# Performance work log

Measured on AMD Instinct MI355X. Metric: run time of the kernel, lower is better.

The kernel has to match this reference:

```python
import jax, jax.numpy as jnp
import numpy as np

NUM_GRAPHS = 32
NODES_PER_GRAPH = 256
N = NUM_GRAPHS * NODES_PER_GRAPH
IN_CH, HID, OUT_CH = 64, 256, 32
K = 20
SPACE, PROP = 3, 2
NEG_SLOPE = 0.01  # F.leaky_relu default
BIG = 1e9         # cross-graph distance mask


def _glorot(key, shape):
    fan_in, fan_out = shape
    lim = (6.0 / (fan_in + fan_out)) ** 0.5
    return jax.random.uniform(key, shape, jnp.float32, -lim, lim)


def setup_inputs() -> dict:
    key = jax.random.key(0)
    ks = jax.random.split(key, 16)
    inp = {
        "x": jax.random.normal(ks[0], (N, IN_CH), jnp.float32),
        "batch": jnp.repeat(jnp.arange(NUM_GRAPHS, dtype=jnp.int32), NODES_PER_GRAPH),
    }
    dims = [(IN_CH, HID), (HID, HID), (HID, OUT_CH)]
    i = 1
    for li, (cin, cout) in enumerate(dims, start=1):
        inp[f"Ws{li}"] = _glorot(ks[i], (cin, SPACE)); i += 1
        inp[f"bs{li}"] = jnp.zeros((SPACE,), jnp.float32)
        inp[f"Wh{li}"] = _glorot(ks[i], (cin, PROP)); i += 1
        inp[f"bh{li}"] = jnp.zeros((PROP,), jnp.float32)
        inp[f"Wo{li}"] = _glorot(ks[i], (cin + PROP, cout)); i += 1
        inp[f"bo{li}"] = jnp.zeros((cout,), jnp.float32)
    return inp


def gravnet_conv(x, mask_add, Ws, bs, Wh, bh, Wo, bo):
    s = x @ Ws + bs                                     # [N,3] learned coords
    h = x @ Wh + bh                                     # [N,2] propagate feats
    s2 = jnp.sum(s * s, axis=1)
    d2 = s2[:, None] + s2[None, :] - 2.0 * (s @ s.T)    # [N,N] squared dists
    d2 = jnp.maximum(d2, 0.0) + mask_add                # block within-graph only
    neg_d2, idx = jax.lax.top_k(-d2, K)                 # kNN (includes self)
    w = jnp.exp(10.0 * neg_d2)                          # exp(-10 * d^2)
    agg = jnp.einsum('nk,nkp->np', w, h[idx])           # aggr='add'
    return jnp.concatenate([agg, x], axis=-1) @ Wo + bo  # lin(cat([out, x]))


def _leaky(h):
    return jnp.where(h >= 0, h, NEG_SLOPE * h)


def reference(x, batch,
              Ws1, bs1, Wh1, bh1, Wo1, bo1,
              Ws2, bs2, Wh2, bh2, Wo2, bo2,
              Ws3, bs3, Wh3, bh3, Wo3, bo3):
    mask_add = jnp.where(batch[:, None] == batch[None, :], 0.0, BIG).astype(x.dtype)
    # dropout p=0.0 -> identity
    h = _leaky(gravnet_conv(x, mask_add, Ws1, bs1, Wh1, bh1, Wo1, bo1))
    h = _leaky(gravnet_conv(h, mask_add, Ws2, bs2, Wh2, bh2, Wo2, bo2))
    out = gravnet_conv(h, mask_add, Ws3, bs3, Wh3, bh3, Wo3, bo3)
    # get_zero_nodes: first node of each contiguous graph segment
    b = jnp.concatenate([jnp.zeros((1,), batch.dtype), batch])
    diff = (b[1:] - b[:-1]).at[0].set(1)
    first_idx = jnp.nonzero(diff != 0, size=NUM_GRAPHS)[0]
    return out[first_idx]
```

## Files before the change

kernel.cpp:

```cpp
#include <hip/hip_runtime.h>
#include <hip/hip_bf16.h>


#define NGRAPH 32
#define GN 256
#define NTOT (NGRAPH*GN)
#define KNN 20
#define CTS 129

typedef __attribute__((ext_vector_type(8))) short bf16x8;
typedef __attribute__((ext_vector_type(4))) float f32x4;

__device__ __forceinline__ ushort f2bf(float x) {
    union { float f; unsigned u; } a; a.f = x;
    unsigned r = a.u + 0x7FFFu + ((a.u >> 16) & 1u);
    return (ushort)(r >> 16);
}
__device__ __forceinline__ float bf2f(ushort h) {
    union { unsigned u; float f; } b; b.u = ((unsigned)h) << 16;
    return b.f;
}
__device__ __forceinline__ bf16x8 ld8(const ushort* p) {
    return *reinterpret_cast<const bf16x8*>(p);
}
__device__ __forceinline__ unsigned pack2(ushort a, ushort b) {
    return (unsigned)a | ((unsigned)b << 16);
}

#define DPP_MIN(v, ctrl, rmask) { \
    unsigned _t = (unsigned)__builtin_amdgcn_update_dpp((int)(v), (int)(v), ctrl, rmask, 0xf, false); \
    (v) = _t < (v) ? _t : (v); }
#define DPP_ADD(v, ctrl, rmask) { \
    float _t = __int_as_float(__builtin_amdgcn_update_dpp(0, __float_as_int(v), ctrl, rmask, 0xf, true)); \
    (v) += _t; }
__device__ __forceinline__ unsigned wave_min_u32(unsigned v) {
    DPP_MIN(v, 0x111, 0xf)
    DPP_MIN(v, 0x112, 0xf)
    DPP_MIN(v, 0x114, 0xf)
    DPP_MIN(v, 0x118, 0xf)
    DPP_MIN(v, 0x142, 0xa)
    DPP_MIN(v, 0x143, 0xc)
    return (unsigned)__builtin_amdgcn_readlane((int)v, 63);
}
__device__ __forceinline__ float wave_sum_f32(float v) {
    DPP_ADD(v, 0x111, 0xf)
    DPP_ADD(v, 0x112, 0xf)
    DPP_ADD(v, 0x114, 0xf)
    DPP_ADD(v, 0x118, 0xf)
    DPP_ADD(v, 0x142, 0xa)
    DPP_ADD(v, 0x143, 0xc)
    return __int_as_float(__builtin_amdgcn_readlane(__float_as_int(v), 63));
}

__device__ __forceinline__ void knn_extract(
    unsigned ua, unsigned ub, unsigned uc, unsigned ud,
    float2 hA, float2 hB, float2 hC, float2 hD,
    int lane, float& out0, float& out1)
{
    float acc0 = 0.f, acc1 = 0.f;
#pragma unroll 1
    for (int it = 0; it < KNN; ++it) {
        unsigned m1 = ua < ub ? ua : ub;
        unsigned m2 = uc < ud ? uc : ud;
        unsigned bv = m1 < m2 ? m1 : m2;
        unsigned gv = wave_min_u32(bv);
        float d2 = __uint_as_float(gv);
        float w = __expf(-10.0f * d2);
        unsigned long long mask = __ballot(bv == gv);
        int wl = __ffsll(mask) - 1;
        if (lane == wl) {
            float h0, h1;
            if (ua == gv)      { h0 = hA.x; h1 = hA.y; ua = 0xFFFFFFFFu; }
            else if (ub == gv) { h0 = hB.x; h1 = hB.y; ub = 0xFFFFFFFFu; }
            else if (uc == gv) { h0 = hC.x; h1 = hC.y; uc = 0xFFFFFFFFu; }
            else               { h0 = hD.x; h1 = hD.y; ud = 0xFFFFFFFFu; }
            acc0 = fmaf(w, h0, acc0);
            acc1 = fmaf(w, h1, acc1);
        }
    }
    out0 = wave_sum_f32(acc0);
    out1 = wave_sum_f32(acc1);
}

__device__ __forceinline__ void knn_rows4(
    const float* sh5, int rbase, int lane, int growbase, float* __restrict__ agg)
{
    float sjx[4], sjy[4], sjz[4], s2j[4];
    float2 hs[4];
#pragma unroll
    for (int t = 0; t < 4; ++t) {
        int j = lane + 64 * t;
        float x = sh5[j * 5 + 0], y = sh5[j * 5 + 1], z = sh5[j * 5 + 2];
        sjx[t] = x; sjy[t] = y; sjz[t] = z;
        s2j[t] = x * x + y * y + z * z;
        hs[t] = make_float2(sh5[j * 5 + 3], sh5[j * 5 + 4]);
    }
    unsigned key[4][4];
    float acc0[4], acc1[4];
#pragma unroll
    for (int r = 0; r < 4; ++r) {
        int rl = rbase + r;
        float s0 = sh5[rl * 5 + 0], s1v = sh5[rl * 5 + 1], s2v = sh5[rl * 5 + 2];
        float s2row = s0 * s0 + s1v * s1v + s2v * s2v;
#pragma unroll
        for (int t = 0; t < 4; ++t) {
            float dot = s0 * sjx[t] + s1v * sjy[t] + s2v * sjz[t];
            float d2 = s2row + s2j[t] - 2.0f * dot;
            key[r][t] = __float_as_uint(d2 > 0.f ? d2 : 0.f);
        }
        acc0[r] = 0.f; acc1[r] = 0.f;
    }
#pragma unroll 1
    for (int it = 0; it < KNN; ++it) {
        unsigned bv[4], gv[4];
#pragma unroll
        for (int r = 0; r < 4; ++r) {
            unsigned m1 = key[r][0] < key[r][1] ? key[r][0] : key[r][1];
            unsigned m2 = key[r][2] < key[r][3] ? key[r][2] : key[r][3];
            bv[r] = m1 < m2 ? m1 : m2;
            gv[r] = bv[r];
        }
#define KSTAGE(ctrl, rmask) { \
        DPP_MIN(gv[0], ctrl, rmask) DPP_MIN(gv[1], ctrl, rmask) \
        DPP_MIN(gv[2], ctrl, rmask) DPP_MIN(gv[3], ctrl, rmask) }
        KSTAGE(0x111, 0xf) KSTAGE(0x112, 0xf) KSTAGE(0x114, 0xf)
        KSTAGE(0x118, 0xf) KSTAGE(0x142, 0xa) KSTAGE(0x143, 0xc)
#undef KSTAGE
#pragma unroll
        for (int r = 0; r < 4; ++r) {
            unsigned g = (unsigned)__builtin_amdgcn_readlane((int)gv[r], 63);
            float w = __expf(-10.0f * __uint_as_float(g));
            unsigned long long mask = __ballot(bv[r] == g);
            int wl = __ffsll(mask) - 1;
            if (lane == wl) {
                float h0, h1;
                if (key[r][0] == g)      { h0 = hs[0].x; h1 = hs[0].y; key[r][0] = 0xFFFFFFFFu; }
                else if (key[r][1] == g) { h0 = hs[1].x; h1 = hs[1].y; key[r][1] = 0xFFFFFFFFu; }
                else if (key[r][2] == g) { h0 = hs[2].x; h1 = hs[2].y; key[r][2] = 0xFFFFFFFFu; }
                else                     { h0 = hs[3].x; h1 = hs[3].y; key[r][3] = 0xFFFFFFFFu; }
                acc0[r] = fmaf(w, h0, acc0[r]);
                acc1[r] = fmaf(w, h1, acc1[r]);
            }
        }
    }
#define SSTAGE(ctrl, rmask) { \
    DPP_ADD(acc0[0], ctrl, rmask) DPP_ADD(acc1[0], ctrl, rmask) \
    DPP_ADD(acc0[1], ctrl, rmask) DPP_ADD(acc1[1], ctrl, rmask) \
    DPP_ADD(acc0[2], ctrl, rmask) DPP_ADD(acc1[2], ctrl, rmask) \
    DPP_ADD(acc0[3], ctrl, rmask) DPP_ADD(acc1[3], ctrl, rmask) }
    SSTAGE(0x111, 0xf) SSTAGE(0x112, 0xf) SSTAGE(0x114, 0xf)
    SSTAGE(0x118, 0xf) SSTAGE(0x142, 0xa) SSTAGE(0x143, 0xc)
#undef SSTAGE
    if (lane == 63) {
#pragma unroll
        for (int r = 0; r < 4; ++r) {
            agg[(growbase + rbase + r) * 2 + 0] = acc0[r];
            agg[(growbase + rbase + r) * 2 + 1] = acc1[r];
        }
    }
}

__global__ __launch_bounds__(256) void knn1_mega(
    const float* __restrict__ X,
    const float* __restrict__ Ws1, const float* __restrict__ bs1,
    const float* __restrict__ Wh1, const float* __restrict__ bh1,
    const float* __restrict__ Wo1, const float* __restrict__ Wo2,
    const float* __restrict__ bs2, const float* __restrict__ bh2,
    const float* __restrict__ bs3, const float* __restrict__ bh3,
    ushort* __restrict__ Wt1hi, ushort* __restrict__ Wt1lo,
    ushort* __restrict__ Wt2hi, ushort* __restrict__ Wt2lo,
    ushort* __restrict__ Xhi, ushort* __restrict__ Xlo,
    float* __restrict__ s2, float* __restrict__ h2p,
    float* __restrict__ s3, float* __restrict__ h3p,
    float* __restrict__ agg)
{
    __shared__ float sh5[256 * 5];
    int b = blockIdx.x, tid = threadIdx.x;
    if (b < 512) {
        int g = b >> 4;
        const float* Xg = X + (size_t)g * (GN * 64);
        {
            float a0 = 0.f, a1 = 0.f, a2 = 0.f, a3 = 0.f, a4 = 0.f;
            const float* xr = Xg + tid * 64;
#pragma unroll 4
            for (int c0 = 0; c0 < 64; c0 += 4) {
                float4 v = *reinterpret_cast<const float4*>(&xr[c0]);
                float xv[4] = {v.x, v.y, v.z, v.w};
#pragma unroll
                for (int j = 0; j < 4; ++j) {
                    int c = c0 + j;
                    a0 = fmaf(xv[j], Ws1[c * 3 + 0], a0);
                    a1 = fmaf(xv[j], Ws1[c * 3 + 1], a1);
                    a2 = fmaf(xv[j], Ws1[c * 3 + 2], a2);
                    a3 = fmaf(xv[j], Wh1[c * 2 + 0], a3);
                    a4 = fmaf(xv[j], Wh1[c * 2 + 1], a4);
                }
            }
            sh5[tid * 5 + 0] = a0 + bs1[0];
            sh5[tid * 5 + 1] = a1 + bs1[1];
            sh5[tid * 5 + 2] = a2 + bs1[2];
            sh5[tid * 5 + 3] = a3 + bh1[0];
            sh5[tid * 5 + 4] = a4 + bh1[1];
        }
        __syncthreads();
        knn_rows4(sh5, (b & 15) * 16 + (tid >> 6) * 4, tid & 63, g * GN, agg);
    } else if (b < 832) {
        int t = (b - 512) * 256 + tid;
        if (t < 65536) {
            int n = t >> 8, c = t & 255;
            float v = Wo2[(size_t)(2 + c) * 256 + n];
            ushort hi = f2bf(v);
            Wt2hi[n * 256 + c] = hi;
            Wt2lo[n * 256 + c] = f2bf(v - bf2f(hi));
        } else {
            int u = t - 65536;
            int n = u >> 6, c = u & 63;
            float v = Wo1[(size_t)(2 + c) * 256 + n];
            ushort hi = f2bf(v);
            Wt1hi[n * 64 + c] = hi;
            Wt1lo[n * 64 + c] = f2bf(v - bf2f(hi));
        }
    } else if (b < 1152) {
        int u = (b - 832) * 256 + tid;
        if (u < 24576)      s2[u] = bs2[u % 3];
        else if (u < 40960) { int w = u - 24576; h2p[w] = bh2[w & 1]; }
        else if (u < 65536) { int w = u - 40960; s3[w] = bs3[w % 3]; }
        else                { int w = u - 65536; h3p[w] = bh3[w & 1]; }
    } else {
        int t = (b - 1152) * 256 + tid;
        float2 v = *reinterpret_cast<const float2*>(&X[(size_t)t * 2]);
        ushort hx = f2bf(v.x), hy = f2bf(v.y);
        Xhi[t * 2 + 0] = hx; Xlo[t * 2 + 0] = f2bf(v.x - bf2f(hx));
        Xhi[t * 2 + 1] = hy; Xlo[t * 2 + 1] = f2bf(v.y - bf2f(hy));
    }
}

__global__ __launch_bounds__(256) void knn2_kernel(
    const float* __restrict__ s, const float* __restrict__ h,
    float* __restrict__ agg)
{
    __shared__ float sh5[256 * 5];
    int b = blockIdx.x, tid = threadIdx.x;
    int g = b & 31, chunk = b >> 5;
    int node = g * GN + tid;
    sh5[tid * 5 + 0] = s[node * 3 + 0];
    sh5[tid * 5 + 1] = s[node * 3 + 1];
    sh5[tid * 5 + 2] = s[node * 3 + 2];
    sh5[tid * 5 + 3] = h[node * 2 + 0];
    sh5[tid * 5 + 4] = h[node * 2 + 1];
    __syncthreads();
    knn_rows4(sh5, chunk * 16 + (tid >> 6) * 4, tid & 63, g * GN, agg);
}

template<int K, int CMODE>
__global__ __launch_bounds__(512) void gemm_fused(
    const ushort* __restrict__ Ahi, const ushort* __restrict__ Alo,
    const ushort* __restrict__ Bhi, const ushort* __restrict__ Blo,
    const float* __restrict__ Wfull, const float* __restrict__ bias,
    const float* __restrict__ agg,
    float* __restrict__ Cf, ushort* __restrict__ Chi, ushort* __restrict__ Clo,
    const float* __restrict__ Wsn, const float* __restrict__ Whn,
    float* __restrict__ s_out, float* __restrict__ h_out)
{
    __shared__ float CT[64 * CTS];
    __shared__ float part[64 * 8 * 5];

    const int tid = threadIdx.x;
    const int lane = tid & 63, wid = tid >> 6;
    const int wm = wid >> 2, wn = wid & 3;
    const int m0 = blockIdx.x * 64, n0 = blockIdx.y * 128;

    f32x4 acc[2][2];
#pragma unroll
    for (int mi = 0; mi < 2; ++mi)
#pragma unroll
        for (int ni = 0; ni < 2; ++ni)
            acc[mi][ni] = (f32x4){0.f, 0.f, 0.f, 0.f};

#pragma unroll 2
    for (int kof = 0; kof < K; kof += 32) {
        int kch = kof + (lane >> 4) * 8;
        bf16x8 ah[2], al[2], bh[2], bl[2];
#pragma unroll
        for (int mi = 0; mi < 2; ++mi) {
            size_t off = (size_t)(m0 + wm * 32 + mi * 16 + (lane & 15)) * K + kch;
            ah[mi] = ld8(Ahi + off); al[mi] = ld8(Alo + off);
        }
#pragma unroll
        for (int ni = 0; ni < 2; ++ni) {
            size_t off = (size_t)(n0 + wn * 32 + ni * 16 + (lane & 15)) * K + kch;
            bh[ni] = ld8(Bhi + off); bl[ni] = ld8(Blo + off);
        }
#pragma unroll
        for (int mi = 0; mi < 2; ++mi)
#pragma unroll
            for (int ni = 0; ni < 2; ++ni) {
                acc[mi][ni] = __builtin_amdgcn_mfma_f32_16x16x32_bf16(ah[mi], bh[ni], acc[mi][ni], 0, 0, 0);
                acc[mi][ni] = __builtin_amdgcn_mfma_f32_16x16x32_bf16(ah[mi], bl[ni], acc[mi][ni], 0, 0, 0);
                acc[mi][ni] = __builtin_amdgcn_mfma_f32_16x16x32_bf16(al[mi], bh[ni], acc[mi][ni], 0, 0, 0);
            }
    }

#pragma unroll
    for (int ni = 0; ni < 2; ++ni) {
        int nl = wn * 32 + ni * 16 + (lane & 15);
        int n = n0 + nl;
        float w0 = Wfull[n], w1 = Wfull[256 + n], bz = bias[n];
#pragma unroll
        for (int mi = 0; mi < 2; ++mi) {
            int mb = wm * 32 + mi * 16 + ((lane >> 4) << 2);
#pragma unroll
            for (int r = 0; r < 4; ++r) {
                int ml = mb + r, m = m0 + ml;
                float v = acc[mi][ni][r] + fmaf(agg[m * 2 + 0], w0, fmaf(agg[m * 2 + 1], w1, bz));
                v = v >= 0.f ? v : 0.01f * v;
                CT[ml * CTS + nl] = v;
                if (CMODE == 1 && (m & 255) == 0) Cf[(m >> 8) * 256 + n] = v;
            }
        }
    }
    __syncthreads();

    if (CMODE == 0) {
        int row = tid >> 3, cbase = (tid & 7) * 16;
        size_t m = (size_t)(m0 + row);
#pragma unroll
        for (int j = 0; j < 2; ++j) {
            int c = cbase + j * 8;
            ushort hi[8], lo[8];
#pragma unroll
            for (int t = 0; t < 8; ++t) {
                float v = CT[row * CTS + c + t];
                hi[t] = f2bf(v);
                lo[t] = f2bf(v - bf2f(hi[t]));
            }
            uint4 wh = make_uint4(pack2(hi[0], hi[1]), pack2(hi[2], hi[3]),
                                  pack2(hi[4], hi[5]), pack2(hi[6], hi[7]));
            uint4 wl = make_uint4(pack2(lo[0], lo[1]), pack2(lo[2], lo[3]),
                                  pack2(lo[4], lo[5]), pack2(lo[6], lo[7]));
            *reinterpret_cast<uint4*>(&Chi[m * 256 + n0 + c]) = wh;
            *reinterpret_cast<uint4*>(&Clo[m * 256 + n0 + c]) = wl;
        }
    }

    {
        int row = tid & 63, sub = tid >> 6;
        float p0 = 0.f, p1 = 0.f, p2 = 0.f, p3 = 0.f, p4 = 0.f;
#pragma unroll
        for (int i = 0; i < 16; ++i) {
            int c = sub * 16 + i;
            float v = CT[row * CTS + c];
            int n = n0 + c;
            p0 = fmaf(v, Wsn[n * 3 + 0], p0);
            p1 = fmaf(v, Wsn[n * 3 + 1], p1);
            p2 = fmaf(v, Wsn[n * 3 + 2], p2);
            p3 = fmaf(v, Whn[n * 2 + 0], p3);
            p4 = fmaf(v, Whn[n * 2 + 1], p4);
        }
        float* pp = &part[(row * 8 + sub) * 5];
        pp[0] = p0; pp[1] = p1; pp[2] = p2; pp[3] = p3; pp[4] = p4;
    }
    __syncthreads();
    if (tid < 320) {
        int row = tid / 5, o = tid - row * 5;
        float sum = 0.f;
#pragma unroll
        for (int k = 0; k < 8; ++k) sum += part[(row * 8 + k) * 5 + o];
        if (o < 3) atomicAdd(&s_out[(m0 + row) * 3 + o], sum);
        else       atomicAdd(&h_out[(m0 + row) * 2 + (o - 3)], sum);
    }
}

__global__ __launch_bounds__(256) void knn3_final(
    const float* __restrict__ s, const float* __restrict__ h,
    const float* __restrict__ h2c,
    const float* __restrict__ Wo, const float* __restrict__ bo,
    float* __restrict__ out)
{
    __shared__ float aggL[2];
    __shared__ float pm[8][32];
    int g = blockIdx.x, tid = threadIdx.x;
    if (tid < 64) {
        int lane = tid;
        int base = g * GN, row = g * GN;
        float s0 = s[row * 3 + 0], s1v = s[row * 3 + 1], s2v = s[row * 3 + 2];
        float s2row = s0 * s0 + s1v * s1v + s2v * s2v;
        unsigned key[4]; float2 hs[4];
#pragma unroll
        for (int t = 0; t < 4; ++t) {
            int j = base + lane + 64 * t;
            float x = s[j * 3 + 0], y = s[j * 3 + 1], z = s[j * 3 + 2];
            float dot = s0 * x + s1v * y + s2v * z;
            float d2 = s2row + (x * x + y * y + z * z) - 2.0f * dot;
            key[t] = __float_as_uint(d2 > 0.f ? d2 : 0.f);
            hs[t] = *reinterpret_cast<const float2*>(&h[(size_t)j * 2]);
        }
        float a0, a1;
        knn_extract(key[0], key[1], key[2], key[3], hs[0], hs[1], hs[2], hs[3], lane, a0, a1);
        if (lane == 63) { aggL[0] = a0; aggL[1] = a1; }
    }
    __syncthreads();
    int o = tid & 31, seg = tid >> 5;
    const float* xr = h2c + g * 256;
    float p = 0.f;
#pragma unroll
    for (int i = 0; i < 32; ++i) {
        int c = seg * 32 + i;
        p = fmaf(xr[c], Wo[(2 + c) * 32 + o], p);
    }
    pm[seg][o] = p;
    __syncthreads();
    if (tid < 32) {
        float acc = fmaf(aggL[0], Wo[o], fmaf(aggL[1], Wo[32 + o], bo[o]));
#pragma unroll
        for (int k = 0; k < 8; ++k) acc += pm[k][o];
        out[g * 32 + o] = acc;
    }
}

extern "C" void kernel_launch(void* const* d_in, const int* in_sizes, int n_in,
                              void* d_out, int out_size, void* d_ws, size_t ws_size,
                              hipStream_t stream) {
    const float* X   = (const float*)d_in[0];
    const float* Ws1 = (const float*)d_in[2];  const float* bs1 = (const float*)d_in[3];
    const float* Wh1 = (const float*)d_in[4];  const float* bh1 = (const float*)d_in[5];
    const float* Wo1 = (const float*)d_in[6];  const float* bo1 = (const float*)d_in[7];
    const float* Ws2 = (const float*)d_in[8];  const float* bs2 = (const float*)d_in[9];
    const float* Wh2 = (const float*)d_in[10]; const float* bh2 = (const float*)d_in[11];
    const float* Wo2 = (const float*)d_in[12]; const float* bo2 = (const float*)d_in[13];
    const float* Ws3 = (const float*)d_in[14]; const float* bs3 = (const float*)d_in[15];
    const float* Wh3 = (const float*)d_in[16]; const float* bh3 = (const float*)d_in[17];
    const float* Wo3 = (const float*)d_in[18]; const float* bo3 = (const float*)d_in[19];

    float* p = (float*)d_ws;
    float* s2   = p; p += NTOT * 3;
    float* hp2  = p; p += NTOT * 2;
    float* s3   = p; p += NTOT * 3;
    float* hp3  = p; p += NTOT * 2;
    float* aggb = p; p += NTOT * 2;
    float* h2c  = p; p += 32 * 256;
    ushort* q = (ushort*)p;
    ushort* Xhi  = q; q += (size_t)NTOT * 64;
    ushort* Xlo  = q; q += (size_t)NTOT * 64;
    ushort* h1hi = q; q += (size_t)NTOT * 256;
    ushort* h1lo = q; q += (size_t)NTOT * 256;
    ushort* Wt1hi = q; q += 256 * 64;
    ushort* Wt1lo = q; q += 256 * 64;
    ushort* Wt2hi = q; q += 256 * 256;
    ushort* Wt2lo = q; q += 256 * 256;

    knn1_mega<<<2176, 256, 0, stream>>>(X, Ws1, bs1, Wh1, bh1, Wo1, Wo2,
                                        bs2, bh2, bs3, bh3,
                                        Wt1hi, Wt1lo, Wt2hi, Wt2lo, Xhi, Xlo,
                                        s2, hp2, s3, hp3, aggb);
    gemm_fused<64, 0><<<dim3(128, 2), 512, 0, stream>>>(Xhi, Xlo, Wt1hi, Wt1lo,
                                                        Wo1, bo1, aggb,
                                                        nullptr, h1hi, h1lo,
                                                        Ws2, Wh2, s2, hp2);
    knn2_kernel<<<512, 256, 0, stream>>>(s2, hp2, aggb);
    gemm_fused<256, 1><<<dim3(128, 2), 512, 0, stream>>>(h1hi, h1lo, Wt2hi, Wt2lo,
                                                         Wo2, bo2, aggb,
                                                         h2c, nullptr, nullptr,
                                                         Ws3, Wh3, s3, hp3);
    knn3_final<<<NGRAPH, 256, 0, stream>>>(s3, hp3, h2c, Wo3, bo3, (float*)d_out);
}
```

Before: 77.13 us.

## Fuse per-layer kNN aggregation with GEMM into single kernels per layer

```diff
diff --git a/kernel.cpp b/kernel.cpp
--- a/kernel.cpp
+++ b/kernel.cpp
@@ -6,7 +6,7 @@
 #define GN 256
 #define NTOT (NGRAPH*GN)
 #define KNN 20
-#define CTS 129
+#define CTS 257
 
 typedef __attribute__((ext_vector_type(8))) short bf16x8;
 typedef __attribute__((ext_vector_type(4))) float f32x4;
@@ -83,7 +83,7 @@
 }
 
 __device__ __forceinline__ void knn_rows4(
-    const float* sh5, int rbase, int lane, int growbase, float* __restrict__ agg)
+    const float* sh5, int srow, int orow, int lane, float* __restrict__ aggL)
 {
     float sjx[4], sjy[4], sjz[4], s2j[4];
     float2 hs[4];
@@ -99,7 +99,7 @@
     float acc0[4], acc1[4];
 #pragma unroll
     for (int r = 0; r < 4; ++r) {
-        int rl = rbase + r;
+        int rl = srow + r;
         float s0 = sh5[rl * 5 + 0], s1v = sh5[rl * 5 + 1], s2v = sh5[rl * 5 + 2];
         float s2row = s0 * s0 + s1v * s1v + s2v * s2v;
 #pragma unroll
@@ -154,179 +154,155 @@
     if (lane == 63) {
 #pragma unroll
         for (int r = 0; r < 4; ++r) {
-            agg[(growbase + rbase + r) * 2 + 0] = acc0[r];
-            agg[(growbase + rbase + r) * 2 + 1] = acc1[r];
-        }
-    }
-}
-
-__global__ __launch_bounds__(256) void knn1_mega(
+            aggL[(orow + r) * 2 + 0] = acc0[r];
+            aggL[(orow + r) * 2 + 1] = acc1[r];
+        }
+    }
+}
+
+__global__ __launch_bounds__(512) void k2_fused(
     const float* __restrict__ X,
     const float* __restrict__ Ws1, const float* __restrict__ bs1,
     const float* __restrict__ Wh1, const float* __restrict__ bh1,
-    const float* __restrict__ Wo1, const float* __restrict__ Wo2,
+    const float* __restrict__ Wo1, const float* __restrict__ bo1,
+    const float* __restrict__ Ws2, const float* __restrict__ Wh2,
     const float* __restrict__ bs2, const float* __restrict__ bh2,
-    const float* __restrict__ bs3, const float* __restrict__ bh3,
-    ushort* __restrict__ Wt1hi, ushort* __restrict__ Wt1lo,
+    const float* __restrict__ Wo2,
     ushort* __restrict__ Wt2hi, ushort* __restrict__ Wt2lo,
-    ushort* __restrict__ Xhi, ushort* __restrict__ Xlo,
-    float* __restrict__ s2, float* __restrict__ h2p,
-    float* __restrict__ s3, float* __restrict__ h3p,
-    float* __restrict__ agg)
+    ushort* __restrict__ h1hi, ushort* __restrict__ h1lo,
+    float* __restrict__ s2, float* __restrict__ hp2)
 {
+    const int x = blockIdx.x, tid = threadIdx.x;
+    if (x >= 128) {
+        int t = (x - 128) * 512 + tid;
+        int n = t >> 8, c = t & 255;
+        float v = Wo2[(size_t)(2 + c) * 256 + n];
+        ushort hi = f2bf(v);
+        Wt2hi[n * 256 + c] = hi;
+        Wt2lo[n * 256 + c] = f2bf(v - bf2f(hi));
+        return;
+    }
     __shared__ float sh5[256 * 5];
-    int b = blockIdx.x, tid = threadIdx.x;
-    if (b < 512) {
-        int g = b >> 4;
-        const float* Xg = X + (size_t)g * (GN * 64);
-        {
-            float a0 = 0.f, a1 = 0.f, a2 = 0.f, a3 = 0.f, a4 = 0.f;
-            const float* xr = Xg + tid * 64;
+    __shared__ float aggL[64 * 2];
+    __shared__ ushort Ahi[64 * 64], Alo[64 * 64];
+    __shared__ float BCT[64 * CTS];
+    __shared__ float part[64 * 8 * 5];
+    ushort* Bhi = (ushort*)BCT;
+    ushort* Blo = Bhi + 256 * 64;
+    float*  CT  = BCT;
+
+    const int lane = tid & 63, wid = tid >> 6;
+    const int g = x >> 2, m0 = x * 64, lr0 = (x & 3) * 64;
+
+    if (tid < 256) {
+        const float* xr = X + ((size_t)g * GN + tid) * 64;
+        float a0 = 0.f, a1 = 0.f, a2 = 0.f, a3 = 0.f, a4 = 0.f;
 #pragma unroll 4
-            for (int c0 = 0; c0 < 64; c0 += 4) {
-                float4 v = *reinterpret_cast<const float4*>(&xr[c0]);
-                float xv[4] = {v.x, v.y, v.z, v.w};
-#pragma unroll
-                for (int j = 0; j < 4; ++j) {
-                    int c = c0 + j;
-                    a0 = fmaf(xv[j], Ws1[c * 3 + 0], a0);
-                    a1 = fmaf(xv[j], Ws1[c * 3 + 1], a1);
-                    a2 = fmaf(xv[j], Ws1[c * 3 + 2], a2);
-                    a3 = fmaf(xv[j], Wh1[c * 2 + 0], a3);
-                    a4 = fmaf(xv[j], Wh1[c * 2 + 1], a4);
-                }
-            }
-            sh5[tid * 5 + 0] = a0 + bs1[0];
-            sh5[tid * 5 + 1] = a1 + bs1[1];
-            sh5[tid * 5 + 2] = a2 + bs1[2];
-            sh5[tid * 5 + 3] = a3 + bh1[0];
-            sh5[tid * 5 + 4] = a4 + bh1[1];
-        }
-        __syncthreads();
-        knn_rows4(sh5, (b & 15) * 16 + (tid >> 6) * 4, tid & 63, g * GN, agg);
-    } else if (b < 832) {
-        int t = (b - 512) * 256 + tid;
-        if (t < 65536) {
-            int n = t >> 8, c = t & 255;
-            float v = Wo2[(size_t)(2 + c) * 256 + n];
-            ushort hi = f2bf(v);
-            Wt2hi[n * 256 + c] = hi;
-            Wt2lo[n * 256 + c] = f2bf(v - bf2f(hi));
-        } else {
-            int u = t - 65536;
-            int n = u >> 6, c = u & 63;
-            float v = Wo1[(size_t)(2 + c) * 256 + n];
-            ushort hi = f2bf(v);
-            Wt1hi[n * 64 + c] = hi;
-            Wt1lo[n * 64 + c] = f2bf(v - bf2f(hi));
-        }
-    } else if (b < 1152) {
-        int u = (b - 832) * 256 + tid;
-        if (u < 24576)      s2[u] = bs2[u % 3];
-        else if (u < 40960) { int w = u - 24576; h2p[w] = bh2[w & 1]; }
-        else if (u < 65536) { int w = u - 40960; s3[w] = bs3[w % 3]; }
-        else                { int w = u - 65536; h3p[w] = bh3[w & 1]; }
-    } else {
-        int t = (b - 1152) * 256 + tid;
-        float2 v = *reinterpret_cast<const float2*>(&X[(size_t)t * 2]);
-        ushort hx = f2bf(v.x), hy = f2bf(v.y);
-        Xhi[t * 2 + 0] = hx; Xlo[t * 2 + 0] = f2bf(v.x - bf2f(hx));
-        Xhi[t * 2 + 1] = hy; Xlo[t * 2 + 1] = f2bf(v.y - bf2f(hy));
-    }
-}
-
-__global__ __launch_bounds__(256) void knn2_kernel(
-    const float* __restrict__ s, const float* __restrict__ h,
-    float* __restrict__ agg)
-{
-    __shared__ float sh5[256 * 5];
-    int b = blockIdx.x, tid = threadIdx.x;
-    int g = b & 31, chunk = b >> 5;
-    int node = g * GN + tid;
-    sh5[tid * 5 + 0] = s[node * 3 + 0];
-    sh5[tid * 5 + 1] = s[node * 3 + 1];
-    sh5[tid * 5 + 2] = s[node * 3 + 2];
-    sh5[tid * 5 + 3] = h[node * 2 + 0];
-    sh5[tid * 5 + 4] = h[node * 2 + 1];
-    __syncthreads();
-    knn_rows4(sh5, chunk * 16 + (tid >> 6) * 4, tid & 63, g * GN, agg);
-}
-
-template<int K, int CMODE>
-__global__ __launch_bounds__(512) void gemm_fused(
-    const ushort* __restrict__ Ahi, const ushort* __restrict__ Alo,
-    const ushort* __restrict__ Bhi, const ushort* __restrict__ Blo,
-    const float* __restrict__ Wfull, const float* __restrict__ bias,
-    const float* __restrict__ agg,
-    float* __restrict__ Cf, ushort* __restrict__ Chi, ushort* __restrict__ Clo,
-    const float* __restrict__ Wsn, const float* __restrict__ Whn,
-    float* __restrict__ s_out, float* __restrict__ h_out)
-{
-    __shared__ float CT[64 * CTS];
-    __shared__ float part[64 * 8 * 5];
-
-    const int tid = threadIdx.x;
-    const int lane = tid & 63, wid = tid >> 6;
+        for (int c0 = 0; c0 < 64; c0 += 4) {
+            float4 v = *reinterpret_cast<const float4*>(&xr[c0]);
+            float xv[4] = {v.x, v.y, v.z, v.w};
+#pragma unroll
+            for (int j = 0; j < 4; ++j) {
+                int c = c0 + j;
+                a0 = fmaf(xv[j], Ws1[c * 3 + 0], a0);
+                a1 = fmaf(xv[j], Ws1[c * 3 + 1], a1);
+                a2 = fmaf(xv[j], Ws1[c * 3 + 2], a2);
+                a3 = fmaf(xv[j], Wh1[c * 2 + 0], a3);
+                a4 = fmaf(xv[j], Wh1[c * 2 + 1], a4);
+            }
+        }
+        sh5[tid * 5 + 0] = a0 + bs1[0];
+        sh5[tid * 5 + 1] = a1 + bs1[1];
+        sh5[tid * 5 + 2] = a2 + bs1[2];
+        sh5[tid * 5 + 3] = a3 + bh1[0];
+        sh5[tid * 5 + 4] = a4 + bh1[1];
+    }
+#pragma unroll
+    for (int i = 0; i < 2; ++i) {
+        int lin = tid + i * 512;
+        int row = lin >> 4, c4 = (lin & 15) * 4;
+        float4 v = *reinterpret_cast<const float4*>(&X[(size_t)(m0 + row) * 64 + c4]);
+        int idx = (row * 64 + c4) ^ ((row & 7) << 3);
+        ushort4 hi, lo;
+        hi.x = f2bf(v.x); lo.x = f2bf(v.x - bf2f(hi.x));
+        hi.y = f2bf(v.y); lo.y = f2bf(v.y - bf2f(hi.y));
+        hi.z = f2bf(v.z); lo.z = f2bf(v.z - bf2f(hi.z));
+        hi.w = f2bf(v.w); lo.w = f2bf(v.w - bf2f(hi.w));
+        *reinterpret_cast<ushort4*>(&Ahi[idx]) = hi;
+        *reinterpret_cast<ushort4*>(&Alo[idx]) = lo;
+    }
+#pragma unroll 4
+    for (int i = 0; i < 32; ++i) {
+        int e = i * 512 + tid;
+        int c = e >> 8, n = e & 255;
+        float v = Wo1[(size_t)(2 + c) * 256 + n];
+        int idx = (n * 64 + c) ^ ((n & 7) << 3);
+        ushort hi = f2bf(v);
+        Bhi[idx] = hi;
+        Blo[idx] = f2bf(v - bf2f(hi));
+    }
+    __syncthreads();
+
+    knn_rows4(sh5, lr0 + wid * 4,      wid * 4,      lane, aggL);
+    knn_rows4(sh5, lr0 + 32 + wid * 4, 32 + wid * 4, lane, aggL);
+
     const int wm = wid >> 2, wn = wid & 3;
-    const int m0 = blockIdx.x * 64, n0 = blockIdx.y * 128;
-
-    f32x4 acc[2][2];
+    f32x4 acc[2][4];
 #pragma unroll
     for (int mi = 0; mi < 2; ++mi)
 #pragma unroll
-        for (int ni = 0; ni < 2; ++ni)
+        for (int ni = 0; ni < 4; ++ni)
             acc[mi][ni] = (f32x4){0.f, 0.f, 0.f, 0.f};
-
-#pragma unroll 2
-    for (int kof = 0; kof < K; kof += 32) {
+#pragma unroll
+    for (int kof = 0; kof < 64; kof += 32) {
         int kch = kof + (lane >> 4) * 8;
-        bf16x8 ah[2], al[2], bh[2], bl[2];
+        bf16x8 ah[2], al[2], bh[4], bl[4];
 #pragma unroll
         for (int mi = 0; mi < 2; ++mi) {
-            size_t off = (size_t)(m0 + wm * 32 + mi * 16 + (lane & 15)) * K + kch;
-            ah[mi] = ld8(Ahi + off); al[mi] = ld8(Alo + off);
-        }
-#pragma unroll
-        for (int ni = 0; ni < 2; ++ni) {
-            size_t off = (size_t)(n0 + wn * 32 + ni * 16 + (lane & 15)) * K + kch;
-            bh[ni] = ld8(Bhi + off); bl[ni] = ld8(Blo + off);
+            int r = wm * 32 + mi * 16 + (lane & 15);
+            int idx = (r * 64 + kch) ^ ((r & 7) << 3);
+            ah[mi] = ld8(&Ahi[idx]); al[mi] = ld8(&Alo[idx]);
+        }
+#pragma unroll
+        for (int ni = 0; ni < 4; ++ni) {
+            int n = wn * 64 + ni * 16 + (lane & 15);
+            int idx = (n * 64 + kch) ^ ((n & 7) << 3);
+            bh[ni] = ld8(&Bhi[idx]); bl[ni] = ld8(&Blo[idx]);
         }
 #pragma unroll
         for (int mi = 0; mi < 2; ++mi)
 #pragma unroll
-            for (int ni = 0; ni < 2; ++ni) {
+            for (int ni = 0; ni < 4; ++ni) {
                 acc[mi][ni] = __builtin_amdgcn_mfma_f32_16x16x32_bf16(ah[mi], bh[ni], acc[mi][ni], 0, 0, 0);
                 acc[mi][ni] = __builtin_amdgcn_mfma_f32_16x16x32_bf16(ah[mi], bl[ni], acc[mi][ni], 0, 0, 0);
                 acc[mi][ni] = __builtin_amdgcn_mfma_f32_16x16x32_bf16(al[mi], bh[ni], acc[mi][ni], 0, 0, 0);
             }
     }
-
-#pragma unroll
-    for (int ni = 0; ni < 2; ++ni) {
-        int nl = wn * 32 + ni * 16 + (lane & 15);
-        int n = n0 + nl;
-        float w0 = Wfull[n], w1 = Wfull[256 + n], bz = bias[n];
+    __syncthreads();
+
+#pragma unroll
+    for (int ni = 0; ni < 4; ++ni) {
+        int n = wn * 64 + ni * 16 + (lane & 15);
+        float w0 = Wo1[n], w1 = Wo1[256 + n], bz = bo1[n];
 #pragma unroll
         for (int mi = 0; mi < 2; ++mi) {
             int mb = wm * 32 + mi * 16 + ((lane >> 4) << 2);
 #pragma unroll
             for (int r = 0; r < 4; ++r) {
-                int ml = mb + r, m = m0 + ml;
-                float v = acc[mi][ni][r] + fmaf(agg[m * 2 + 0], w0, fmaf(agg[m * 2 + 1], w1, bz));
-                v = v >= 0.f ? v : 0.01f * v;
-                CT[ml * CTS + nl] = v;
-                if (CMODE == 1 && (m & 255) == 0) Cf[(m >> 8) * 256 + n] = v;
-            }
-        }
-    }
-    __syncthreads();
-
-    if (CMODE == 0) {
-        int row = tid >> 3, cbase = (tid & 7) * 16;
+                int ml = mb + r;
+                float v = acc[mi][ni][r] + fmaf(aggL[ml * 2 + 0], w0, fmaf(aggL[ml * 2 + 1], w1, bz));
+                CT[ml * CTS + n] = v >= 0.f ? v : 0.01f * v;
+            }
+        }
+    }
+    __syncthreads();
+
+    {
+        int row = tid >> 3, cb = (tid & 7) * 32;
         size_t m = (size_t)(m0 + row);
 #pragma unroll
-        for (int j = 0; j < 2; ++j) {
-            int c = cbase + j * 8;
+        for (int j = 0; j < 4; ++j) {
+            int c = cb + j * 8;
             ushort hi[8], lo[8];
 #pragma unroll
             for (int t = 0; t < 8; ++t) {
@@ -338,24 +314,22 @@
                                   pack2(hi[4], hi[5]), pack2(hi[6], hi[7]));
             uint4 wl = make_uint4(pack2(lo[0], lo[1]), pack2(lo[2], lo[3]),
                                   pack2(lo[4], lo[5]), pack2(lo[6], lo[7]));
-            *reinterpret_cast<uint4*>(&Chi[m * 256 + n0 + c]) = wh;
-            *reinterpret_cast<uint4*>(&Clo[m * 256 + n0 + c]) = wl;
-        }
-    }
-
+            *reinterpret_cast<uint4*>(&h1hi[m * 256 + c]) = wh;
+            *reinterpret_cast<uint4*>(&h1lo[m * 256 + c]) = wl;
+        }
+    }
     {
         int row = tid & 63, sub = tid >> 6;
         float p0 = 0.f, p1 = 0.f, p2 = 0.f, p3 = 0.f, p4 = 0.f;
 #pragma unroll
-        for (int i = 0; i < 16; ++i) {
-            int c = sub * 16 + i;
+        for (int i = 0; i < 32; ++i) {
+            int c = sub * 32 + i;
             float v = CT[row * CTS + c];
-            int n = n0 + c;
-            p0 = fmaf(v, Wsn[n * 3 + 0], p0);
-            p1 = fmaf(v, Wsn[n * 3 + 1], p1);
-            p2 = fmaf(v, Wsn[n * 3 + 2], p2);
-            p3 = fmaf(v, Whn[n * 2 + 0], p3);
-            p4 = fmaf(v, Whn[n * 2 + 1], p4);
+            p0 = fmaf(v, Ws2[c * 3 + 0], p0);
+            p1 = fmaf(v, Ws2[c * 3 + 1], p1);
+            p2 = fmaf(v, Ws2[c * 3 + 2], p2);
+            p3 = fmaf(v, Wh2[c * 2 + 0], p3);
+            p4 = fmaf(v, Wh2[c * 2 + 1], p4);
         }
         float* pp = &part[(row * 8 + sub) * 5];
         pp[0] = p0; pp[1] = p1; pp[2] = p2; pp[3] = p3; pp[4] = p4;
@@ -366,8 +340,116 @@
         float sum = 0.f;
 #pragma unroll
         for (int k = 0; k < 8; ++k) sum += part[(row * 8 + k) * 5 + o];
-        if (o < 3) atomicAdd(&s_out[(m0 + row) * 3 + o], sum);
-        else       atomicAdd(&h_out[(m0 + row) * 2 + (o - 3)], sum);
+        if (o < 3) s2[(m0 + row) * 3 + o] = bs2[o] + sum;
+        else       hp2[(m0 + row) * 2 + (o - 3)] = bh2[o - 3] + sum;
+    }
+}
+
+__global__ __launch_bounds__(512) void k3_fused(
+    const float* __restrict__ s2, const float* __restrict__ hp2,
+    const ushort* __restrict__ h1hi, const ushort* __restrict__ h1lo,
+    const ushort* __restrict__ Wt2hi, const ushort* __restrict__ Wt2lo,
+    const float* __restrict__ Wo2, const float* __restrict__ bo2,
+    const float* __restrict__ Ws3, const float* __restrict__ Wh3,
+    const float* __restrict__ bs3, const float* __restrict__ bh3,
+    float* __restrict__ h2c, float* __restrict__ s3, float* __restrict__ hp3)
+{
+    __shared__ float sh5[256 * 5];
+    __shared__ float aggL[64 * 2];
+    __shared__ float CT[64 * CTS];
+    __shared__ float part[64 * 8 * 5];
+
+    const int x = blockIdx.x, tid = threadIdx.x;
+    const int lane = tid & 63, wid = tid >> 6;
+    const int g = x >> 2, m0 = x * 64, lr0 = (x & 3) * 64;
+
+    if (tid < 256) {
+        int node = g * GN + tid;
+        sh5[tid * 5 + 0] = s2[node * 3 + 0];
+        sh5[tid * 5 + 1] = s2[node * 3 + 1];
+        sh5[tid * 5 + 2] = s2[node * 3 + 2];
+        sh5[tid * 5 + 3] = hp2[node * 2 + 0];
+        sh5[tid * 5 + 4] = hp2[node * 2 + 1];
+    }
+    __syncthreads();
+    knn_rows4(sh5, lr0 + wid * 4,      wid * 4,      lane, aggL);
+    knn_rows4(sh5, lr0 + 32 + wid * 4, 32 + wid * 4, lane, aggL);
+    __syncthreads();
+
+    const int wm = wid >> 2, wn = wid & 3;
+    f32x4 acc[2][4];
+#pragma unroll
+    for (int mi = 0; mi < 2; ++mi)
+#pragma unroll
+        for (int ni = 0; ni < 4; ++ni)
+            acc[mi][ni] = (f32x4){0.f, 0.f, 0.f, 0.f};
+#pragma unroll 2
+    for (int kof = 0; kof < 256; kof += 32) {
+        int kch = kof + (lane >> 4) * 8;
+        bf16x8 ah[2], al[2], bh[4], bl[4];
+#pragma unroll
+        for (int mi = 0; mi < 2; ++mi) {
+            size_t off = (size_t)(m0 + wm * 32 + mi * 16 + (lane & 15)) * 256 + kch;
+            ah[mi] = ld8(h1hi + off); al[mi] = ld8(h1lo + off);
+        }
+#pragma unroll
+        for (int ni = 0; ni < 4; ++ni) {
+            size_t off = (size_t)(wn * 64 + ni * 16 + (lane & 15)) * 256 + kch;
+            bh[ni] = ld8(Wt2hi + off); bl[ni] = ld8(Wt2lo + off);
+        }
+#pragma unroll
+        for (int mi = 0; mi < 2; ++mi)
+#pragma unroll
+            for (int ni = 0; ni < 4; ++ni) {
+                acc[mi][ni] = __builtin_amdgcn_mfma_f32_16x16x32_bf16(ah[mi], bh[ni], acc[mi][ni], 0, 0, 0);
+                acc[mi][ni] = __builtin_amdgcn_mfma_f32_16x16x32_bf16(ah[mi], bl[ni], acc[mi][ni], 0, 0, 0);
+                acc[mi][ni] = __builtin_amdgcn_mfma_f32_16x16x32_bf16(al[mi], bh[ni], acc[mi][ni], 0, 0, 0);
+            }
+    }
+
+#pragma unroll
+    for (int ni = 0; ni < 4; ++ni) {
+        int n = wn * 64 + ni * 16 + (lane & 15);
+        float w0 = Wo2[n], w1 = Wo2[256 + n], bz = bo2[n];
+#pragma unroll
+        for (int mi = 0; mi < 2; ++mi) {
+            int mb = wm * 32 + mi * 16 + ((lane >> 4) << 2);
+#pragma unroll
+            for (int r = 0; r < 4; ++r) {
+                int ml = mb + r;
+                float v = acc[mi][ni][r] + fmaf(aggL[ml * 2 + 0], w0, fmaf(aggL[ml * 2 + 1], w1, bz));
+                CT[ml * CTS + n] = v >= 0.f ? v : 0.01f * v;
+            }
+        }
+    }
+    __syncthreads();
+
+    if ((x & 3) == 0 && tid < 256) h2c[g * 256 + tid] = CT[tid];
+
+    {
+        int row = tid & 63, sub = tid >> 6;
+        float p0 = 0.f, p1 = 0.f, p2 = 0.f, p3 = 0.f, p4 = 0.f;
+#pragma unroll
+        for (int i = 0; i < 32; ++i) {
+            int c = sub * 32 + i;
+            float v = CT[row * CTS + c];
+            p0 = fmaf(v, Ws3[c * 3 + 0], p0);
+            p1 = fmaf(v, Ws3[c * 3 + 1], p1);
+            p2 = fmaf(v, Ws3[c * 3 + 2], p2);
+            p3 = fmaf(v, Wh3[c * 2 + 0], p3);
+            p4 = fmaf(v, Wh3[c * 2 + 1], p4);
+        }
+        float* pp = &part[(row * 8 + sub) * 5];
+        pp[0] = p0; pp[1] = p1; pp[2] = p2; pp[3] = p3; pp[4] = p4;
+    }
+    __syncthreads();
+    if (tid < 320) {
+        int row = tid / 5, o = tid - row * 5;
+        float sum = 0.f;
+#pragma unroll
+        for (int k = 0; k < 8; ++k) sum += part[(row * 8 + k) * 5 + o];
+        if (o < 3) s3[(m0 + row) * 3 + o] = bs3[o] + sum;
+        else       hp3[(m0 + row) * 2 + (o - 3)] = bh3[o - 3] + sum;
     }
 }
 
@@ -389,9 +471,9 @@
 #pragma unroll
         for (int t = 0; t < 4; ++t) {
             int j = base + lane + 64 * t;
-            float x = s[j * 3 + 0], y = s[j * 3 + 1], z = s[j * 3 + 2];
-            float dot = s0 * x + s1v * y + s2v * z;
-            float d2 = s2row + (x * x + y * y + z * z) - 2.0f * dot;
+            float xx = s[j * 3 + 0], y = s[j * 3 + 1], z = s[j * 3 + 2];
+            float dot = s0 * xx + s1v * y + s2v * z;
+            float d2 = s2row + (xx * xx + y * y + z * z) - 2.0f * dot;
             key[t] = __float_as_uint(d2 > 0.f ? d2 : 0.f);
             hs[t] = *reinterpret_cast<const float2*>(&h[(size_t)j * 2]);
         }
@@ -437,30 +519,18 @@
     float* hp2  = p; p += NTOT * 2;
     float* s3   = p; p += NTOT * 3;
     float* hp3  = p; p += NTOT * 2;
-    float* aggb = p; p += NTOT * 2;
     float* h2c  = p; p += 32 * 256;
     ushort* q = (ushort*)p;
-    ushort* Xhi  = q; q += (size_t)NTOT * 64;
-    ushort* Xlo  = q; q += (size_t)NTOT * 64;
     ushort* h1hi = q; q += (size_t)NTOT * 256;
     ushort* h1lo = q; q += (size_t)NTOT * 256;
-    ushort* Wt1hi = q; q += 256 * 64;
-    ushort* Wt1lo = q; q += 256 * 64;
     ushort* Wt2hi = q; q += 256 * 256;
     ushort* Wt2lo = q; q += 256 * 256;
 
-    knn1_mega<<<2176, 256, 0, stream>>>(X, Ws1, bs1, Wh1, bh1, Wo1, Wo2,
-                                        bs2, bh2, bs3, bh3,
-                                        Wt1hi, Wt1lo, Wt2hi, Wt2lo, Xhi, Xlo,
-                                        s2, hp2, s3, hp3, aggb);
-    gemm_fused<64, 0><<<dim3(128, 2), 512, 0, stream>>>(Xhi, Xlo, Wt1hi, Wt1lo,
-                                                        Wo1, bo1, aggb,
-                                                        nullptr, h1hi, h1lo,
-                                                        Ws2, Wh2, s2, hp2);
-    knn2_kernel<<<512, 256, 0, stream>>>(s2, hp2, aggb);
-    gemm_fused<256, 1><<<dim3(128, 2), 512, 0, stream>>>(h1hi, h1lo, Wt2hi, Wt2lo,
-                                                         Wo2, bo2, aggb,
-                                                         h2c, nullptr, nullptr,
-                                                         Ws3, Wh3, s3, hp3);
+    k2_fused<<<256, 512, 0, stream>>>(X, Ws1, bs1, Wh1, bh1, Wo1, bo1,
+                                      Ws2, Wh2, bs2, bh2, Wo2,
+                                      Wt2hi, Wt2lo, h1hi, h1lo, s2, hp2);
+    k3_fused<<<128, 512, 0, stream>>>(s2, hp2, h1hi, h1lo, Wt2hi, Wt2lo,
+                                      Wo2, bo2, Ws3, Wh3, bs3, bh3,
+                                      h2c, s3, hp3);
     knn3_final<<<NGRAPH, 256, 0, stream>>>(s3, hp3, h2c, Wo3, bo3, (float*)d_out);
 }
```

Measured after the change: 110.0 us. +42.6%, slower.
